# Kernel optimization log

Measured on AMD Instinct MI355X. Metric: run time of the kernel, lower is better.

The kernel has to match this reference:

```python
import jax, jax.numpy as jnp
import numpy as np

Q_MAX = 127.0  # 2^(8-1) - 1 for 8-bit activations


def _ste_round(x):
    # forward: round(x); backward: identity
    return x + jax.lax.stop_gradient(jnp.round(x) - x)


def setup_inputs() -> dict:
    key = jax.random.key(0)
    k1, k2 = jax.random.split(key)
    B, S, D_IN, D_OUT = 4, 4096, 2048, 2048
    x = jax.random.normal(k1, (B, S, D_IN), dtype=jnp.float32)
    # muP-style init: std = 1/sqrt(fan_in)
    weight = jax.random.normal(k2, (D_OUT, D_IN), dtype=jnp.float32) / np.sqrt(D_IN)
    return {"x": x, "weight": weight}


def reference(x, weight):
    # --- ternary weight quantization (AbsMean) ---
    w_scale = jnp.maximum(jnp.mean(jnp.abs(weight)), 1e-6)        # scalar
    w_norm = weight / w_scale
    w_quant = jnp.clip(_ste_round(w_norm), -1.0, 1.0)             # [O, I], values in {-1,0,1}

    # --- per-token absmax activation quantization (8-bit) ---
    a_scale = jnp.clip(jnp.max(jnp.abs(x), axis=-1, keepdims=True), 1e-8, None)  # [B,S,1]
    x_quant = jnp.clip(_ste_round(x * (Q_MAX / a_scale)), -Q_MAX, Q_MAX)         # [B,S,I]

    # --- scaled matmul: y = (x_q @ w_q^T) * w_scale * (a_scale / Q_MAX) ---
    y = jnp.einsum('bsi,oi->bso', x_quant, w_quant)
    y = y * (w_scale * (a_scale / Q_MAX))
    return y
```

## Files before the change

### kernel.cpp

```cpp
#include <hip/hip_runtime.h>
#include <hip/hip_bf16.h>

typedef int int4v __attribute__((ext_vector_type(4)));

#define K_DIM 2048
#define N_DIM 2048
#define M_DIM 16384
#define NW 4194304
#define BKB 128
#define NKT (K_DIM / BKB)

__global__ void k_wsum(const float4* __restrict__ w4, double* __restrict__ red) {
  const int n4 = NW / 4;
  double s = 0.0;
  for (int i = blockIdx.x * blockDim.x + threadIdx.x; i < n4; i += gridDim.x * blockDim.x) {
    float4 v = w4[i];
    s += (double)fabsf(v.x) + (double)fabsf(v.y) + (double)fabsf(v.z) + (double)fabsf(v.w);
  }
  for (int o = 32; o; o >>= 1) s += __shfl_xor(s, o);
  __shared__ double sd[4];
  if ((threadIdx.x & 63) == 0) sd[threadIdx.x >> 6] = s;
  __syncthreads();
  if (threadIdx.x == 0) red[blockIdx.x] = (sd[0] + sd[1]) + (sd[2] + sd[3]);
}

__global__ void k_wscale(const double* __restrict__ red, double* __restrict__ wsd) {
  double s = red[threadIdx.x];
  for (int o = 32; o; o >>= 1) s += __shfl_xor(s, o);
  __shared__ double sd[4];
  if ((threadIdx.x & 63) == 0) sd[threadIdx.x >> 6] = s;
  __syncthreads();
  if (threadIdx.x == 0) {
    double m = ((sd[0] + sd[1]) + (sd[2] + sd[3])) / (double)NW;
    *wsd = (m > 1e-6) ? m : 1e-6;
  }
}

__device__ __forceinline__ char wq1(float v, double ws) {
  double r = rint((double)v / ws);
  r = fmin(fmax(r, -1.0), 1.0);
  return (char)(int)r;
}

__global__ void k_wquant(const float4* __restrict__ w4, const double* __restrict__ wsd,
                         char4* __restrict__ wq4) {
  int i = blockIdx.x * blockDim.x + threadIdx.x;
  if (i >= NW / 4) return;
  double ws = *wsd;
  float4 v = w4[i];
  char4 q;
  q.x = wq1(v.x, ws);
  q.y = wq1(v.y, ws);
  q.z = wq1(v.z, ws);
  q.w = wq1(v.w, ws);
  wq4[i] = q;
}

__device__ __forceinline__ char qi8(float v, double rr) {
  double q = rint((double)v * rr);
  q = fmin(fmax(q, -127.0), 127.0);
  return (char)(int)q;
}

__global__ void k_xquant(const float* __restrict__ x, float* __restrict__ ascale,
                         char* __restrict__ xq) {
  const int row = blockIdx.x;
  const int t = threadIdx.x;
  const float4* xr = (const float4*)(x + (size_t)row * K_DIM);
  float4 v0 = xr[t];
  float4 v1 = xr[t + 256];
  float m = fmaxf(fmaxf(fmaxf(fabsf(v0.x), fabsf(v0.y)), fmaxf(fabsf(v0.z), fabsf(v0.w))),
                  fmaxf(fmaxf(fabsf(v1.x), fabsf(v1.y)), fmaxf(fabsf(v1.z), fabsf(v1.w))));
  for (int o = 32; o; o >>= 1) m = fmaxf(m, __shfl_xor(m, o));
  __shared__ float sm[4];
  if ((t & 63) == 0) sm[t >> 6] = m;
  __syncthreads();
  float a = fmaxf(fmaxf(sm[0], sm[1]), fmaxf(sm[2], sm[3]));
  a = fmaxf(a, 1e-8f);
  if (t == 0) ascale[row] = a;
  double rr = 127.0 / (double)a;
  char4* qr4 = (char4*)(xq + (size_t)row * K_DIM);
  char4 a4, b4;
  a4.x = qi8(v0.x, rr); a4.y = qi8(v0.y, rr); a4.z = qi8(v0.z, rr); a4.w = qi8(v0.w, rr);
  b4.x = qi8(v1.x, rr); b4.y = qi8(v1.y, rr); b4.z = qi8(v1.z, rr); b4.w = qi8(v1.w, rr);
  qr4[t] = a4;
  qr4[t + 256] = b4;
}

__device__ __forceinline__ void gload16(const void* g, void* l) {
  __builtin_amdgcn_global_load_lds(
      (const __attribute__((address_space(1))) void*)g,
      (__attribute__((address_space(3))) void*)l, 16, 0, 0);
}

#define RD_A(DST, CA, MH, CO)                                               \
  _Pragma("unroll") for (int mf = 0; mf < 4; ++mf)                          \
    DST[mf] = *(const int4v*)((CA) + (rA + (MH)*64 + mf * 16) * 128 + (CO));

#define RD_B(DST, CB, CO)                                                   \
  _Pragma("unroll") for (int nf = 0; nf < 4; ++nf)                          \
    DST[nf] = *(const int4v*)((CB) + (rB + nf * 16) * 128 + (CO));

#define MM(MH, AF, BF)                                                      \
  __builtin_amdgcn_s_setprio(1);                                            \
  _Pragma("unroll") for (int mf = 0; mf < 4; ++mf)                          \
  _Pragma("unroll") for (int nf = 0; nf < 4; ++nf)                          \
    acc[(MH)*4 + mf][nf] = __builtin_amdgcn_mfma_i32_16x16x64_i8(           \
        AF[mf], BF[nf], acc[(MH)*4 + mf][nf], 0, 0, 0);                     \
  __builtin_amdgcn_s_setprio(0);

#define CFENCE asm volatile("" ::: "memory")
#define BAR    do { CFENCE; __builtin_amdgcn_s_barrier(); CFENCE; } while (0)
#define LGKM0  do { asm volatile("s_waitcnt lgkmcnt(0)" ::: "memory");      \
                    __builtin_amdgcn_sched_barrier(0); } while (0)

#define KTILE(KT, CA, CB, NA, NB)                                           \
  {                                                                         \
    const char* An = Ab + (((KT) + 1) & (NKT - 1)) * BKB;                   \
    const char* Bn = Bb + (((KT) + 1) & (NKT - 1)) * BKB;                   \
                          \
    RD_A(afA, CA, 0, co0);                                                  \
    RD_B(bfA, CB, co0);                                                     \
    _Pragma("unroll") for (int c = 0; c < 4; ++c)                           \
      gload16(An + soff[c], (NA) + loff[c]);                                \
    BAR; LGKM0;                                                             \
    MM(0, afA, bfA);                                                        \
    BAR;                                                                    \
               \
    RD_A(afB, CA, 1, co0);                                                  \
    _Pragma("unroll") for (int c = 0; c < 4; ++c)                           \
      gload16(Bn + soff[c], (NB) + loff[c]);                                \
    BAR; LGKM0;                                                             \
    MM(1, afB, bfA);                                                        \
    BAR;                                                                    \
                                          \
    RD_A(afA, CA, 0, co1);                                                  \
    RD_B(bfB, CB, co1);                                                     \
    BAR; LGKM0;                                                             \
    MM(0, afA, bfB);                                                        \
    BAR;                                                                    \
                \
    RD_A(afB, CA, 1, co1);                                                  \
    BAR; LGKM0;                                                             \
    MM(1, afB, bfB);                                                        \
    asm volatile("s_waitcnt vmcnt(0)" ::: "memory");                        \
    BAR;                                                                    \
  }

__global__ __launch_bounds__(512, 1) void k_gemm(
    const char* __restrict__ xq, const char* __restrict__ wq,
    const float* __restrict__ ascale, const double* __restrict__ wsd,
    float* __restrict__ out) {
  __shared__ __align__(16) char lds[131072];
  char* lA0 = lds;
  char* lB0 = lds + 32768;
  char* lA1 = lds + 65536;
  char* lB1 = lds + 98304;

  const int tid = threadIdx.x;
  const int l = tid & 63;
  const int wv = tid >> 6;
  const int wm = wv >> 2;
  const int wn = wv & 3;
  const int g = l >> 4, r16 = l & 15;

  const int bid = blockIdx.x;
  const int logical = (bid & 7) * 64 + (bid >> 3);
  const int br = logical >> 3;
  const int bc = logical & 7;

  const char* Ab = xq + (size_t)br * 256 * K_DIM;
  const char* Bb = wq + (size_t)bc * 256 * K_DIM;

  int soff[4], loff[4];
#pragma unroll
  for (int c = 0; c < 4; ++c) {
    int lb = c * 8192 + tid * 16;
    loff[c] = lb;
    int row = lb >> 7;
    int cb = lb & 127;
    soff[c] = row * K_DIM + (cb ^ ((row & 7) << 4));
  }

  const int sw = (r16 & 7) << 4;
  const int co0 = (g * 16) ^ sw;
  const int co1 = (64 + g * 16) ^ sw;
  const int rA = wm * 128 + r16;
  const int rB = wn * 64 + r16;

  int4v acc[8][4];
#pragma unroll
  for (int mf = 0; mf < 8; ++mf)
#pragma unroll
    for (int nf = 0; nf < 4; ++nf) acc[mf][nf] = (int4v){0, 0, 0, 0};

#pragma unroll
  for (int c = 0; c < 4; ++c) gload16(Ab + soff[c], lA0 + loff[c]);
#pragma unroll
  for (int c = 0; c < 4; ++c) gload16(Bb + soff[c], lB0 + loff[c]);
  asm volatile("s_waitcnt vmcnt(0)" ::: "memory");
  BAR;

  int4v afA[4], afB[4], bfA[4], bfB[4];

  for (int kt = 0; kt < NKT; kt += 2) {
    KTILE(kt,     lA0, lB0, lA1, lB1);
    KTILE(kt + 1, lA1, lB1, lA0, lB0);
  }

  float wsf = (float)(*wsd);
  size_t trow0 = (size_t)br * 256 + wm * 128;
  int oc0 = bc * 256 + wn * 64;
#pragma unroll
  for (int mf = 0; mf < 8; ++mf) {
#pragma unroll
    for (int j = 0; j < 4; ++j) {
      size_t t = trow0 + mf * 16 + g * 4 + j;
      float s = wsf * (ascale[t] / 127.0f);
      float* yr = out + t * (size_t)N_DIM + oc0;
#pragma unroll
      for (int nf = 0; nf < 4; ++nf) yr[nf * 16 + r16] = (float)acc[mf][nf][j] * s;
    }
  }
}

extern "C" void kernel_launch(void* const* d_in, const int* in_sizes, int n_in,
                              void* d_out, int out_size, void* d_ws, size_t ws_size,
                              hipStream_t stream) {
  const float* x = (const float*)d_in[0];
  const float* w = (const float*)d_in[1];
  float* out = (float*)d_out;

  char* ws = (char*)d_ws;
  double* red = (double*)ws;
  double* wsd = (double*)(ws + 2048);
  float* ascale = (float*)(ws + 4096);
  char* xq = (char*)(ws + 4096 + 65536);
  char* wq = xq + (size_t)M_DIM * K_DIM;

  k_wsum<<<256, 256, 0, stream>>>((const float4*)w, red);
  k_wscale<<<1, 256, 0, stream>>>(red, wsd);
  k_wquant<<<NW / 4 / 256, 256, 0, stream>>>((const float4*)w, wsd, (char4*)wq);
  k_xquant<<<M_DIM, 256, 0, stream>>>(x, ascale, xq);
  k_gemm<<<dim3(N_DIM / 256 * M_DIM / 256), 512, 0, stream>>>(xq, wq, ascale, wsd, out);
}
```

Before: 128.2 us.

## Software-pipeline LDS fragment reads one step ahead of MFMA blocks

Restructures the K-tile loop so each LDS fragment read is issued one phase before the MFMA block that uses it, and the next tile's first A/B fragments are prefetched during the last MFMA block. The explicit lgkmcnt(0) waits and sched_barriers are removed, leaving the compiler to insert waits. The goal is to hide LDS read latency behind matrix instructions. In exchange it relies on compiler-inserted waitcnts and adds a prologue read before the loop.

```diff
diff --git a/kernel.cpp b/kernel.cpp
--- a/kernel.cpp
+++ b/kernel.cpp
@@ -111,39 +111,37 @@
 
 #define CFENCE asm volatile("" ::: "memory")
 #define BAR    do { CFENCE; __builtin_amdgcn_s_barrier(); CFENCE; } while (0)
-#define LGKM0  do { asm volatile("s_waitcnt lgkmcnt(0)" ::: "memory");      \
-                    __builtin_amdgcn_sched_barrier(0); } while (0)
-
-#define KTILE(KT, CA, CB, NA, NB)                                           \
+
+#define TILE(CA, CB, NA, NB, KT)                                            \
   {                                                                         \
     const char* An = Ab + (((KT) + 1) & (NKT - 1)) * BKB;                   \
     const char* Bn = Bb + (((KT) + 1) & (NKT - 1)) * BKB;                   \
-                          \
-    RD_A(afA, CA, 0, co0);                                                  \
-    RD_B(bfA, CB, co0);                                                     \
+        \
+    RD_A(afY, CA, 1, co0);                                                  \
     _Pragma("unroll") for (int c = 0; c < 4; ++c)                           \
       gload16(An + soff[c], (NA) + loff[c]);                                \
-    BAR; LGKM0;                                                             \
-    MM(0, afA, bfA);                                                        \
-    BAR;                                                                    \
-               \
-    RD_A(afB, CA, 1, co0);                                                  \
+    BAR;                                                                    \
+    MM(0, afX, bfP);                                                        \
+    BAR;                                                                    \
+       \
+    RD_A(afX, CA, 0, co1);                                                  \
+    RD_B(bfQ, CB, co1);                                                     \
     _Pragma("unroll") for (int c = 0; c < 4; ++c)                           \
       gload16(Bn + soff[c], (NB) + loff[c]);                                \
-    BAR; LGKM0;                                                             \
-    MM(1, afB, bfA);                                                        \
-    BAR;                                                                    \
-                                          \
-    RD_A(afA, CA, 0, co1);                                                  \
-    RD_B(bfB, CB, co1);                                                     \
-    BAR; LGKM0;                                                             \
-    MM(0, afA, bfB);                                                        \
-    BAR;                                                                    \
-                \
-    RD_A(afB, CA, 1, co1);                                                  \
-    BAR; LGKM0;                                                             \
-    MM(1, afB, bfB);                                                        \
+    BAR;                                                                    \
+    MM(1, afY, bfP);                                                        \
+    BAR;                                                                    \
+                        \
+    RD_A(afY, CA, 1, co1);                                                  \
+    BAR;                                                                    \
+    MM(0, afX, bfQ);                                                        \
+    BAR;                                                                    \
+        \
     asm volatile("s_waitcnt vmcnt(0)" ::: "memory");                        \
+    BAR;                \
+    RD_A(afX, NA, 0, co0);                                                  \
+    RD_B(bfP, NB, co0);                                                     \
+    MM(1, afY, bfQ);                                                        \
     BAR;                                                                    \
   }
 
@@ -201,11 +199,18 @@
   asm volatile("s_waitcnt vmcnt(0)" ::: "memory");
   BAR;
 
-  int4v afA[4], afB[4], bfA[4], bfB[4];
+  int4v afA0[4], afA1[4], bfB0[4], bfB1[4];
+#define afX afA0
+#define afY afA1
+#define bfP bfB0
+#define bfQ bfB1
+
+  RD_A(afX, lA0, 0, co0);
+  RD_B(bfP, lB0, co0);
 
   for (int kt = 0; kt < NKT; kt += 2) {
-    KTILE(kt,     lA0, lB0, lA1, lB1);
-    KTILE(kt + 1, lA1, lB1, lA0, lB0);
+    TILE(lA0, lB0, lA1, lB1, kt);
+    TILE(lA1, lB1, lA0, lB0, kt + 1);
   }
 
   float wsf = (float)(*wsd);
```

Result: no change. 127.4 us (-0.6%).
